# Kernel optimization log

Measured on AMD Instinct MI355X. Metric: run time of the kernel, lower is better.

Reference implementation:

```python
import jax, jax.numpy as jnp
import numpy as np

NUM_EXPERTS = 8
TOP_K = 2


def setup_inputs() -> dict:
    key = jax.random.key(0)
    ks = jax.random.split(key, 6)
    B, S, D, H, E = 4, 1024, 1024, 2048, NUM_EXPERTS
    x = jax.random.normal(ks[0], (B, S, D), dtype=jnp.float32)
    Wg = jax.random.normal(ks[1], (D, E), dtype=jnp.float32) * 0.02
    W1 = jax.random.normal(ks[2], (E, D, H), dtype=jnp.float32) * 0.02
    b1 = jax.random.normal(ks[3], (E, H), dtype=jnp.float32) * 0.02
    W2 = jax.random.normal(ks[4], (E, H, D), dtype=jnp.float32) * 0.02
    b2 = jax.random.normal(ks[5], (E, D), dtype=jnp.float32) * 0.02
    return {"x": x, "Wg": Wg, "W1": W1, "b1": b1, "W2": W2, "b2": b2}


def reference(x, Wg, W1, b1, W2, b2):
    B, S, D = x.shape
    E, _, H = W1.shape
    OUT = W2.shape[2]
    xm = x.reshape(-1, D)                      # [N, D], N = B*S
    # --- top-k gating (ProbabilitySamplerTopk): softmax over experts, take top-k ---
    logits = xm @ Wg                           # [N, E]
    probs = jax.nn.softmax(logits, axis=-1)
    topk_p, topk_i = jax.lax.top_k(probs, TOP_K)   # [N, K]
    # --- sort dispatched (token, expert) pairs by expert id (stable) ---
    flat_e = topk_i.reshape(-1)                # [N*K]
    flat_p = topk_p.reshape(-1)                # [N*K]
    order = jnp.argsort(flat_e)                # stable sort -> grouped by expert
    tok_idx = order // TOP_K                   # source token index (trunc-div by topK)
    e_sorted = flat_e[order]                   # [N*K]
    p_sorted = flat_p[order]                   # [N*K]
    xs = xm[tok_idx]                           # [N*K, D] expert-sorted inputs
    # --- grouped-GEMM experts: masked per-expert dense GEMM (E is small & fixed) ---
    y = jnp.zeros((xs.shape[0], OUT), dtype=xs.dtype)
    for e in range(E):
        h = jax.nn.relu(xs @ W1[e] + b1[e])    # [N*K, H]
        ye = h @ W2[e] + b2[e]                 # [N*K, OUT]
        m = (e_sorted == e)[:, None].astype(xs.dtype)
        y = y + m * ye
    # --- combine: multiply by gates, scatter-add back to token slots ---
    y = y * p_sorted[:, None]
    out = jnp.zeros((B * S, OUT), dtype=y.dtype).at[tok_idx].add(y)
    return out.reshape(B, S, OUT)
```

## Files before the change

### kernel.cpp

```cpp
#include <hip/hip_runtime.h>
#include <hip/hip_bf16.h>
#include <stdint.h>

typedef __bf16 bf16;
typedef __bf16 bf16x8 __attribute__((ext_vector_type(8)));
typedef __bf16 bf16x4 __attribute__((ext_vector_type(4)));
typedef float f32x4 __attribute__((ext_vector_type(4)));

#define N_TOK 4096
#define DDIM 1024
#define HDIM 2048
#define NPAIR 8192

__device__ __forceinline__ void gload16(const void* g, void* l) {
  __builtin_amdgcn_global_load_lds(
      (const __attribute__((address_space(1))) unsigned int*)g,
      (__attribute__((address_space(3))) unsigned int*)l, 16, 0, 0);
}

__global__ void transpose_cvt_kernel(const float* __restrict__ in, bf16* __restrict__ out,
                                     int R, int C) {
  __shared__ float tile[32][33];
  const float* ip = in + (size_t)blockIdx.z * R * C;
  bf16* op = out + (size_t)blockIdx.z * R * C;
  int r0 = blockIdx.y * 32, c0 = blockIdx.x * 32;
  int tr = threadIdx.x >> 3;
  int tc = (threadIdx.x & 7) * 4;
  float4 v = *(const float4*)(ip + (size_t)(r0 + tr) * C + c0 + tc);
  tile[tr][tc] = v.x; tile[tr][tc + 1] = v.y; tile[tr][tc + 2] = v.z; tile[tr][tc + 3] = v.w;
  __syncthreads();
  bf16x4 o = {(bf16)tile[tc + 0][tr], (bf16)tile[tc + 1][tr],
              (bf16)tile[tc + 2][tr], (bf16)tile[tc + 3][tr]};
  *(bf16x4*)(op + (size_t)(c0 + tr) * R + r0 + tc) = o;
}

__global__ void gate_kernel(const float* __restrict__ x, const float* __restrict__ Wg,
                            int2* __restrict__ ge, float2* __restrict__ gp,
                            bf16* __restrict__ xb, float* __restrict__ outp) {
  int t0 = blockIdx.x * 4;
  {
    float4 z = make_float4(0.f, 0.f, 0.f, 0.f);
    float4* ob = (float4*)(outp + (size_t)t0 * DDIM);
#pragma unroll
    for (int r = 0; r < 4; r++) ob[r * 256 + threadIdx.x] = z;
  }
  int t = t0 + (threadIdx.x >> 6);
  int lane = threadIdx.x & 63;
  const float* xr = x + (size_t)t * DDIM;
  bf16* xbr = xb + (size_t)t * DDIM;
  float a[8];
#pragma unroll
  for (int e = 0; e < 8; e++) a[e] = 0.f;
#pragma unroll
  for (int it = 0; it < 4; it++) {
    int d0 = it * 256 + lane * 4;
    float4 xv = *(const float4*)(xr + d0);
    bf16x4 o = {(bf16)xv.x, (bf16)xv.y, (bf16)xv.z, (bf16)xv.w};
    *(bf16x4*)(xbr + d0) = o;
    float xs[4] = {xv.x, xv.y, xv.z, xv.w};
#pragma unroll
    for (int dd = 0; dd < 4; dd++) {
      float4 w0 = *(const float4*)(Wg + (size_t)(d0 + dd) * 8);
      float4 w1 = *(const float4*)(Wg + (size_t)(d0 + dd) * 8 + 4);
      a[0] += xs[dd] * w0.x; a[1] += xs[dd] * w0.y; a[2] += xs[dd] * w0.z; a[3] += xs[dd] * w0.w;
      a[4] += xs[dd] * w1.x; a[5] += xs[dd] * w1.y; a[6] += xs[dd] * w1.z; a[7] += xs[dd] * w1.w;
    }
  }
#pragma unroll
  for (int off = 32; off >= 1; off >>= 1) {
#pragma unroll
    for (int e = 0; e < 8; e++) a[e] += __shfl_xor(a[e], off);
  }
  if (lane == 0) {
    float m = a[0];
#pragma unroll
    for (int e = 1; e < 8; e++) m = fmaxf(m, a[e]);
    float p[8]; float s = 0.f;
#pragma unroll
    for (int e = 0; e < 8; e++) { p[e] = expf(a[e] - m); s += p[e]; }
    float inv = 1.f / s;
    int i0 = 0; float v0 = a[0];
#pragma unroll
    for (int e = 1; e < 8; e++) if (a[e] > v0) { v0 = a[e]; i0 = e; }
    int i1 = -1; float v1 = -1e30f;
#pragma unroll
    for (int e = 0; e < 8; e++) if (e != i0 && a[e] > v1) { v1 = a[e]; i1 = e; }
    ge[t] = make_int2(i0, i1);
    gp[t] = make_float2(p[i0] * inv, p[i1] * inv);
  }
}

__global__ void sort_kernel(const int2* __restrict__ ge, const float2* __restrict__ gp,
                            int* __restrict__ tok, float* __restrict__ ps,
                            int* __restrict__ meta) {
  __shared__ int hist[8], runn[8], wc[16][8], wb[16][8], baseS[9];
  int tid = threadIdx.x;
  int lane = tid & 63, wv = tid >> 6;
  if (tid < 8) hist[tid] = 0;
  __syncthreads();
  for (int i = tid; i < NPAIR; i += 1024) {
    int2 g = ge[i >> 1];
    int e = (i & 1) ? g.y : g.x;
    atomicAdd(&hist[e], 1);
  }
  __syncthreads();
  if (tid == 0) {
    int b = 0, ts1 = 0;
    for (int e = 0; e < 8; e++) {
      baseS[e] = b; meta[e] = b;
      meta[9 + e] = ts1;  ts1 += (hist[e] + 127) / 128;
      b += hist[e];
    }
    baseS[8] = b; meta[8] = b; meta[17] = ts1;
  }
  __syncthreads();
  if (tid < 8) runn[tid] = baseS[tid];
  __syncthreads();
  for (int c = 0; c < 8; c++) {
    int i = c * 1024 + tid;
    int2 g = ge[i >> 1];
    int e = (i & 1) ? g.y : g.x;
    int rank = 0;
#pragma unroll
    for (int ee = 0; ee < 8; ee++) {
      unsigned long long b = __ballot(e == ee);
      if (e == ee) rank = __popcll(b & ((1ull << lane) - 1ull));
      if (lane == 0) wc[wv][ee] = __popcll(b);
    }
    __syncthreads();
    if (tid < 8) {
      int s = runn[tid];
      for (int w = 0; w < 16; w++) { wb[w][tid] = s; s += wc[w][tid]; }
      runn[tid] = s;
    }
    __syncthreads();
    int pos = wb[wv][e] + rank;
    tok[pos] = i >> 1;
    float2 p2 = gp[i >> 1];
    ps[pos] = (i & 1) ? p2.y : p2.x;
    __syncthreads();
  }
}

template <int KDIM, int NPE, bool FIRST, int NT>
__global__ __launch_bounds__(256, 4)
void moe_gemm_kernel(const bf16* __restrict__ A, const bf16* __restrict__ Bt,
                     const float* __restrict__ bias, const int* __restrict__ tok,
                     const float* __restrict__ ps, const int* __restrict__ meta,
                     bf16* __restrict__ hout, float* __restrict__ outp) {
  __shared__ bf16 lds[2][8192];
  constexpr int nk = KDIM / 32;

  int MTa = meta[17];
  int xcd = blockIdx.x & 7;
  int idx = blockIdx.x >> 3;
  int mLo = (MTa * xcd) >> 3;
  int mHi = (MTa * (xcd + 1)) >> 3;
  int cnt = mHi - mLo;
  if (idx >= cnt * NT) return;
  int tileN = idx / cnt;
  int tileM = mLo + idx - tileN * cnt;

  int e = 0;
#pragma unroll
  for (int k = 1; k < 8; k++) if (tileM >= meta[9 + k]) e = k;
  int row0 = meta[e] + (tileM - meta[9 + e]) * 128;
  int segEnd = meta[e + 1];
  int n0 = tileN * 128;

  int t = threadIdx.x;
  const bf16* aSrc[2];
  const bf16* bSrc[2];
  {
    int swz = ((t & 3) ^ ((t >> 3) & 3)) * 8;
#pragma unroll
    for (int r = 0; r < 2; r++) {
      int row = r * 64 + (t >> 2);
      int gRow = row0 + row; if (gRow > NPAIR - 1) gRow = NPAIR - 1;
      int arow = FIRST ? tok[gRow] : gRow;
      aSrc[r] = A + (size_t)arow * KDIM + swz;
      bSrc[r] = Bt + ((size_t)e * NPE + n0 + row) * KDIM + swz;
    }
  }

  int lane = t & 63, wv = t >> 6;
  int wm = wv >> 1, wn = wv & 1;
  int l15 = lane & 15, l4 = lane >> 4;
  int aOff[4], bOff[4];
#pragma unroll
  for (int m = 0; m < 4; m++) {
    int row = wm * 64 + m * 16 + l15;
    aOff[m] = row * 32 + ((l4 ^ ((row >> 1) & 3)) * 8);
  }
#pragma unroll
  for (int n = 0; n < 4; n++) {
    int row = wn * 64 + n * 16 + l15;
    bOff[n] = 4096 + row * 32 + ((l4 ^ ((row >> 1) & 3)) * 8);
  }

  f32x4 acc[4][4];
#pragma unroll
  for (int m = 0; m < 4; m++)
#pragma unroll
    for (int n = 0; n < 4; n++)
#pragma unroll
      for (int j = 0; j < 4; j++) acc[m][n][j] = 0.f;

  auto STAGE = [&](int kt, int buf) {
    bf16* sb = &lds[buf][0];
    int ko = kt * 32;
    gload16(aSrc[0] + ko, sb + t * 8);
    gload16(aSrc[1] + ko, sb + 2048 + t * 8);
    gload16(bSrc[0] + ko, sb + 4096 + t * 8);
    gload16(bSrc[1] + ko, sb + 6144 + t * 8);
  };

  STAGE(0, 0);
  __syncthreads();

  for (int kt = 0; kt < nk; kt++) {
    if (kt + 1 < nk) STAGE(kt + 1, (kt + 1) & 1);
    const bf16* sb = &lds[kt & 1][0];
    bf16x8 af[4], bfr[4];
#pragma unroll
    for (int m = 0; m < 4; m++) af[m] = *(const bf16x8*)(sb + aOff[m]);
#pragma unroll
    for (int n = 0; n < 4; n++) bfr[n] = *(const bf16x8*)(sb + bOff[n]);
#pragma unroll
    for (int m = 0; m < 4; m++)
#pragma unroll
      for (int n = 0; n < 4; n++)
        acc[m][n] = __builtin_amdgcn_mfma_f32_16x16x32_bf16(af[m], bfr[n], acc[m][n], 0, 0, 0);
    __syncthreads();
  }

  int colb = n0 + wn * 64 + l15;
  int rowb = wm * 64 + l4 * 4;
  float bia[4];
#pragma unroll
  for (int n = 0; n < 4; n++) bia[n] = bias[(size_t)e * NPE + colb + n * 16];
#pragma unroll
  for (int m = 0; m < 4; m++) {
#pragma unroll
    for (int jj = 0; jj < 4; jj++) {
      int gRow = row0 + rowb + m * 16 + jj;
      if (gRow < segEnd) {
        if (FIRST) {
#pragma unroll
          for (int n = 0; n < 4; n++) {
            float v = acc[m][n][jj] + bia[n];
            v = fmaxf(v, 0.f);
            hout[(size_t)gRow * NPE + colb + n * 16] = (bf16)v;
          }
        } else {
          float pscale = ps[gRow];
          float* orow = outp + (size_t)tok[gRow] * DDIM;
#pragma unroll
          for (int n = 0; n < 4; n++) {
            float v = (acc[m][n][jj] + bia[n]) * pscale;
            atomicAdd(orow + colb + n * 16, v);
          }
        }
      }
    }
  }
}

extern "C" void kernel_launch(void* const* d_in, const int* in_sizes, int n_in,
                              void* d_out, int out_size, void* d_ws, size_t ws_size,
                              hipStream_t stream) {
  (void)in_sizes; (void)n_in; (void)out_size; (void)ws_size;
  const float* x  = (const float*)d_in[0];
  const float* Wg = (const float*)d_in[1];
  const float* W1 = (const float*)d_in[2];
  const float* b1 = (const float*)d_in[3];
  const float* W2 = (const float*)d_in[4];
  const float* b2 = (const float*)d_in[5];
  float* out = (float*)d_out;

  char* ws = (char*)d_ws;
  bf16*  xb   = (bf16*)(ws);
  bf16*  W1T  = (bf16*)(ws + (8ull  << 20));
  bf16*  W2T  = (bf16*)(ws + (40ull << 20));
  bf16*  hbuf = (bf16*)(ws + (72ull << 20));
  char*  ext  = ws + (104ull << 20);
  int2*   ge      = (int2*)(ext);
  float2* gp      = (float2*)(ext + (64u  << 10));
  int*    tok     = (int*)(ext + (128u << 10));
  float*  psarr   = (float*)(ext + (160u << 10));
  int*    meta    = (int*)(ext + (224u << 10));

  transpose_cvt_kernel<<<dim3(64, 32, 8), 256, 0, stream>>>(W1, W1T, 1024, 2048);
  transpose_cvt_kernel<<<dim3(32, 64, 8), 256, 0, stream>>>(W2, W2T, 2048, 1024);
  gate_kernel<<<1024, 256, 0, stream>>>(x, Wg, ge, gp, xb, out);
  sort_kernel<<<1, 1024, 0, stream>>>(ge, gp, tok, psarr, meta);
  moe_gemm_kernel<1024, 2048, true, 16><<<dim3(1152), 256, 0, stream>>>(
      xb, W1T, b1, tok, psarr, meta, hbuf, nullptr);
  moe_gemm_kernel<2048, 1024, false, 8><<<dim3(576), 256, 0, stream>>>(
      hbuf, W2T, b2, tok, psarr, meta, nullptr, out);
}
```

Before: 194.5 us.

## Split second GEMM along K into two halves and load B directly from global

The second expert GEMM is split along K into two halves, which doubles its grid to the same block count as the first GEMM. Each half accumulates via atomics into its own fp32 buffer, and a new combine kernel adds the two buffers into the output. Both GEMMs now read B fragments straight from global memory into registers instead of staging them through LDS. This halves LDS use and the launch bound drops to 3 blocks. The trade-off is uncoalesced global B loads inside the inner loop, extra zeroing of two buffers, and an extra combine pass over the output.

After: 322.8 us. 1.66x slower.

```diff
diff --git a/kernel.cpp b/kernel.cpp
--- a/kernel.cpp
+++ b/kernel.cpp
@@ -36,13 +36,18 @@
 
 __global__ void gate_kernel(const float* __restrict__ x, const float* __restrict__ Wg,
                             int2* __restrict__ ge, float2* __restrict__ gp,
-                            bf16* __restrict__ xb, float* __restrict__ outp) {
+                            bf16* __restrict__ xb, float* __restrict__ y2a,
+                            float* __restrict__ y2b) {
   int t0 = blockIdx.x * 4;
   {
     float4 z = make_float4(0.f, 0.f, 0.f, 0.f);
-    float4* ob = (float4*)(outp + (size_t)t0 * DDIM);
-#pragma unroll
-    for (int r = 0; r < 4; r++) ob[r * 256 + threadIdx.x] = z;
+    float4* za = (float4*)(y2a + (size_t)t0 * DDIM);
+    float4* zb = (float4*)(y2b + (size_t)t0 * DDIM);
+#pragma unroll
+    for (int r = 0; r < 4; r++) {
+      za[r * 256 + threadIdx.x] = z;
+      zb[r * 256 + threadIdx.x] = z;
+    }
   }
   int t = t0 + (threadIdx.x >> 6);
   int lane = threadIdx.x & 63;
@@ -142,14 +147,19 @@
   }
 }
 
-template <int KDIM, int NPE, bool FIRST, int NT>
-__global__ __launch_bounds__(256, 4)
+template <bool FIRST>
+__global__ __launch_bounds__(256, 3)
 void moe_gemm_kernel(const bf16* __restrict__ A, const bf16* __restrict__ Bt,
                      const float* __restrict__ bias, const int* __restrict__ tok,
                      const float* __restrict__ ps, const int* __restrict__ meta,
-                     bf16* __restrict__ hout, float* __restrict__ outp) {
-  __shared__ bf16 lds[2][8192];
-  constexpr int nk = KDIM / 32;
+                     bf16* __restrict__ hout, float* __restrict__ y2a,
+                     float* __restrict__ y2b) {
+  constexpr int AKst = FIRST ? DDIM : HDIM;
+  constexpr int BKst = FIRST ? DDIM : HDIM;
+  constexpr int NPE  = FIRST ? HDIM : DDIM;
+  constexpr int NT   = 16;
+  constexpr int nk   = 32;
+  __shared__ bf16 lds[2][4096];
 
   int MTa = meta[17];
   int xcd = blockIdx.x & 7;
@@ -166,11 +176,12 @@
   for (int k = 1; k < 8; k++) if (tileM >= meta[9 + k]) e = k;
   int row0 = meta[e] + (tileM - meta[9 + e]) * 128;
   int segEnd = meta[e + 1];
-  int n0 = tileN * 128;
+  int n0, kOff;
+  if (FIRST) { n0 = tileN * 128; kOff = 0; }
+  else       { n0 = (tileN & 7) * 128; kOff = (tileN >> 3) * 1024; }
 
   int t = threadIdx.x;
   const bf16* aSrc[2];
-  const bf16* bSrc[2];
   {
     int swz = ((t & 3) ^ ((t >> 3) & 3)) * 8;
 #pragma unroll
@@ -178,24 +189,24 @@
       int row = r * 64 + (t >> 2);
       int gRow = row0 + row; if (gRow > NPAIR - 1) gRow = NPAIR - 1;
       int arow = FIRST ? tok[gRow] : gRow;
-      aSrc[r] = A + (size_t)arow * KDIM + swz;
-      bSrc[r] = Bt + ((size_t)e * NPE + n0 + row) * KDIM + swz;
+      aSrc[r] = A + (size_t)arow * AKst + kOff + swz;
     }
   }
 
   int lane = t & 63, wv = t >> 6;
   int wm = wv >> 1, wn = wv & 1;
   int l15 = lane & 15, l4 = lane >> 4;
-  int aOff[4], bOff[4];
+  int aOff[4];
 #pragma unroll
   for (int m = 0; m < 4; m++) {
     int row = wm * 64 + m * 16 + l15;
     aOff[m] = row * 32 + ((l4 ^ ((row >> 1) & 3)) * 8);
   }
+  const bf16* bBase[4];
 #pragma unroll
   for (int n = 0; n < 4; n++) {
     int row = wn * 64 + n * 16 + l15;
-    bOff[n] = 4096 + row * 32 + ((l4 ^ ((row >> 1) & 3)) * 8);
+    bBase[n] = Bt + ((size_t)e * NPE + n0 + row) * BKst + kOff + l4 * 8;
   }
 
   f32x4 acc[4][4];
@@ -206,26 +217,24 @@
 #pragma unroll
       for (int j = 0; j < 4; j++) acc[m][n][j] = 0.f;
 
-  auto STAGE = [&](int kt, int buf) {
+  auto STAGE_A = [&](int kt, int buf) {
     bf16* sb = &lds[buf][0];
     int ko = kt * 32;
     gload16(aSrc[0] + ko, sb + t * 8);
     gload16(aSrc[1] + ko, sb + 2048 + t * 8);
-    gload16(bSrc[0] + ko, sb + 4096 + t * 8);
-    gload16(bSrc[1] + ko, sb + 6144 + t * 8);
   };
 
-  STAGE(0, 0);
+  STAGE_A(0, 0);
   __syncthreads();
 
   for (int kt = 0; kt < nk; kt++) {
-    if (kt + 1 < nk) STAGE(kt + 1, (kt + 1) & 1);
+    if (kt + 1 < nk) STAGE_A(kt + 1, (kt + 1) & 1);
     const bf16* sb = &lds[kt & 1][0];
     bf16x8 af[4], bfr[4];
 #pragma unroll
+    for (int n = 0; n < 4; n++) bfr[n] = *(const bf16x8*)(bBase[n] + kt * 32);
+#pragma unroll
     for (int m = 0; m < 4; m++) af[m] = *(const bf16x8*)(sb + aOff[m]);
-#pragma unroll
-    for (int n = 0; n < 4; n++) bfr[n] = *(const bf16x8*)(sb + bOff[n]);
 #pragma unroll
     for (int m = 0; m < 4; m++)
 #pragma unroll
@@ -238,7 +247,9 @@
   int rowb = wm * 64 + l4 * 4;
   float bia[4];
 #pragma unroll
-  for (int n = 0; n < 4; n++) bia[n] = bias[(size_t)e * NPE + colb + n * 16];
+  for (int n = 0; n < 4; n++)
+    bia[n] = (FIRST || kOff == 0) ? bias[(size_t)e * NPE + colb + n * 16] : 0.f;
+  float* ybuf = FIRST ? nullptr : ((kOff == 0) ? y2a : y2b);
 #pragma unroll
   for (int m = 0; m < 4; m++) {
 #pragma unroll
@@ -250,11 +261,11 @@
           for (int n = 0; n < 4; n++) {
             float v = acc[m][n][jj] + bia[n];
             v = fmaxf(v, 0.f);
-            hout[(size_t)gRow * NPE + colb + n * 16] = (bf16)v;
+            hout[(size_t)gRow * HDIM + colb + n * 16] = (bf16)v;
           }
         } else {
           float pscale = ps[gRow];
-          float* orow = outp + (size_t)tok[gRow] * DDIM;
+          float* orow = ybuf + (size_t)tok[gRow] * DDIM;
 #pragma unroll
           for (int n = 0; n < 4; n++) {
             float v = (acc[m][n][jj] + bia[n]) * pscale;
@@ -264,6 +275,14 @@
       }
     }
   }
+}
+
+__global__ void combine_kernel(const float* __restrict__ a, const float* __restrict__ b,
+                               float* __restrict__ out) {
+  int i = blockIdx.x * 256 + threadIdx.x;
+  f32x4 va = ((const f32x4*)a)[i];
+  f32x4 vb = ((const f32x4*)b)[i];
+  ((f32x4*)out)[i] = va + vb;
 }
 
 extern "C" void kernel_launch(void* const* d_in, const int* in_sizes, int n_in,
@@ -283,7 +302,9 @@
   bf16*  W1T  = (bf16*)(ws + (8ull  << 20));
   bf16*  W2T  = (bf16*)(ws + (40ull << 20));
   bf16*  hbuf = (bf16*)(ws + (72ull << 20));
-  char*  ext  = ws + (104ull << 20);
+  float* y2a  = (float*)(ws + (104ull << 20));
+  float* y2b  = (float*)(ws + (120ull << 20));
+  char*  ext  = ws + (136ull << 20);
   int2*   ge      = (int2*)(ext);
   float2* gp      = (float2*)(ext + (64u  << 10));
   int*    tok     = (int*)(ext + (128u << 10));
@@ -292,10 +313,11 @@
 
   transpose_cvt_kernel<<<dim3(64, 32, 8), 256, 0, stream>>>(W1, W1T, 1024, 2048);
   transpose_cvt_kernel<<<dim3(32, 64, 8), 256, 0, stream>>>(W2, W2T, 2048, 1024);
-  gate_kernel<<<1024, 256, 0, stream>>>(x, Wg, ge, gp, xb, out);
+  gate_kernel<<<1024, 256, 0, stream>>>(x, Wg, ge, gp, xb, y2a, y2b);
   sort_kernel<<<1, 1024, 0, stream>>>(ge, gp, tok, psarr, meta);
-  moe_gemm_kernel<1024, 2048, true, 16><<<dim3(1152), 256, 0, stream>>>(
-      xb, W1T, b1, tok, psarr, meta, hbuf, nullptr);
-  moe_gemm_kernel<2048, 1024, false, 8><<<dim3(576), 256, 0, stream>>>(
-      hbuf, W2T, b2, tok, psarr, meta, nullptr, out);
-}
+  moe_gemm_kernel<true><<<dim3(1152), 256, 0, stream>>>(
+      xb, W1T, b1, tok, psarr, meta, hbuf, nullptr, nullptr);
+  moe_gemm_kernel<false><<<dim3(1152), 256, 0, stream>>>(
+      hbuf, W2T, b2, tok, psarr, meta, nullptr, y2a, y2b);
+  combine_kernel<<<4096, 256, 0, stream>>>(y2a, y2b, out);
+}
```

## Use 32x32x16 MFMA in expert GEMMs and widen transpose tiles to 64x64

Applied to the files above, without the earlier changes.

The grouped expert GEMM inner loop moves from 16x16x32 bf16 MFMA instructions to 32x32x16 ones, so each wave issues four larger MFMAs per k-substep from fewer LDS fragment loads. The epilogue is remapped to the 32x32 accumulator layout. Separately, the weight transpose/convert kernel now processes 64x64 tiles per block and writes 16-byte bf16x8 stores. This reduces LDS read traffic per FLOP and improves transpose store width, at the cost of a larger LDS tile and a more complex output index mapping.

Result: slower. 205.1 us (+5.5%).

```diff
diff --git a/kernel.cpp b/kernel.cpp
--- a/kernel.cpp
+++ b/kernel.cpp
@@ -6,6 +6,7 @@
 typedef __bf16 bf16x8 __attribute__((ext_vector_type(8)));
 typedef __bf16 bf16x4 __attribute__((ext_vector_type(4)));
 typedef float f32x4 __attribute__((ext_vector_type(4)));
+typedef float f32x16 __attribute__((ext_vector_type(16)));
 
 #define N_TOK 4096
 #define DDIM 1024
@@ -18,20 +19,34 @@
       (__attribute__((address_space(3))) unsigned int*)l, 16, 0, 0);
 }
 
-__global__ void transpose_cvt_kernel(const float* __restrict__ in, bf16* __restrict__ out,
-                                     int R, int C) {
-  __shared__ float tile[32][33];
+__global__ __launch_bounds__(256)
+void transpose_cvt_kernel(const float* __restrict__ in, bf16* __restrict__ out,
+                          int R, int C) {
+  __shared__ float tile[64][65];
   const float* ip = in + (size_t)blockIdx.z * R * C;
   bf16* op = out + (size_t)blockIdx.z * R * C;
-  int r0 = blockIdx.y * 32, c0 = blockIdx.x * 32;
-  int tr = threadIdx.x >> 3;
-  int tc = (threadIdx.x & 7) * 4;
-  float4 v = *(const float4*)(ip + (size_t)(r0 + tr) * C + c0 + tc);
-  tile[tr][tc] = v.x; tile[tr][tc + 1] = v.y; tile[tr][tc + 2] = v.z; tile[tr][tc + 3] = v.w;
-  __syncthreads();
-  bf16x4 o = {(bf16)tile[tc + 0][tr], (bf16)tile[tc + 1][tr],
-              (bf16)tile[tc + 2][tr], (bf16)tile[tc + 3][tr]};
-  *(bf16x4*)(op + (size_t)(c0 + tr) * R + r0 + tc) = o;
+  int c0 = blockIdx.x * 64, r0 = blockIdx.y * 64;
+  int t = threadIdx.x;
+  int ir = t >> 2;
+  int icb = (t & 3) * 16;
+#pragma unroll
+  for (int j = 0; j < 4; j++) {
+    float4 v = *(const float4*)(ip + (size_t)(r0 + ir) * C + c0 + icb + j * 4);
+    tile[ir][icb + j * 4 + 0] = v.x;
+    tile[ir][icb + j * 4 + 1] = v.y;
+    tile[ir][icb + j * 4 + 2] = v.z;
+    tile[ir][icb + j * 4 + 3] = v.w;
+  }
+  __syncthreads();
+  int oc = t >> 2;
+  int orb = (t & 3) * 16;
+#pragma unroll
+  for (int s = 0; s < 2; s++) {
+    bf16x8 o;
+#pragma unroll
+    for (int q = 0; q < 8; q++) o[q] = (bf16)tile[orb + s * 8 + q][oc];
+    *(bf16x8*)(op + (size_t)(c0 + oc) * R + r0 + orb + s * 8) = o;
+  }
 }
 
 __global__ void gate_kernel(const float* __restrict__ x, const float* __restrict__ Wg,
@@ -185,26 +200,26 @@
 
   int lane = t & 63, wv = t >> 6;
   int wm = wv >> 1, wn = wv & 1;
-  int l15 = lane & 15, l4 = lane >> 4;
-  int aOff[4], bOff[4];
-#pragma unroll
-  for (int m = 0; m < 4; m++) {
-    int row = wm * 64 + m * 16 + l15;
-    aOff[m] = row * 32 + ((l4 ^ ((row >> 1) & 3)) * 8);
-  }
-#pragma unroll
-  for (int n = 0; n < 4; n++) {
-    int row = wn * 64 + n * 16 + l15;
-    bOff[n] = 4096 + row * 32 + ((l4 ^ ((row >> 1) & 3)) * 8);
-  }
-
-  f32x4 acc[4][4];
-#pragma unroll
-  for (int m = 0; m < 4; m++)
-#pragma unroll
-    for (int n = 0; n < 4; n++)
-#pragma unroll
-      for (int j = 0; j < 4; j++) acc[m][n][j] = 0.f;
+  int l31 = lane & 31, l5 = lane >> 5;
+  int aOff[2][2], bOff[2][2];
+#pragma unroll
+  for (int f = 0; f < 2; f++)
+#pragma unroll
+    for (int ks = 0; ks < 2; ks++) {
+      int arow = wm * 64 + f * 32 + l31;
+      int brow = wn * 64 + f * 32 + l31;
+      int kc = ks * 2 + l5;
+      aOff[f][ks] = arow * 32 + ((kc ^ ((arow >> 1) & 3)) * 8);
+      bOff[f][ks] = 4096 + brow * 32 + ((kc ^ ((brow >> 1) & 3)) * 8);
+    }
+
+  f32x16 acc[2][2];
+#pragma unroll
+  for (int m = 0; m < 2; m++)
+#pragma unroll
+    for (int n = 0; n < 2; n++)
+#pragma unroll
+      for (int j = 0; j < 16; j++) acc[m][n][j] = 0.f;
 
   auto STAGE = [&](int kt, int buf) {
     bf16* sb = &lds[buf][0];
@@ -221,44 +236,49 @@
   for (int kt = 0; kt < nk; kt++) {
     if (kt + 1 < nk) STAGE(kt + 1, (kt + 1) & 1);
     const bf16* sb = &lds[kt & 1][0];
-    bf16x8 af[4], bfr[4];
-#pragma unroll
-    for (int m = 0; m < 4; m++) af[m] = *(const bf16x8*)(sb + aOff[m]);
-#pragma unroll
-    for (int n = 0; n < 4; n++) bfr[n] = *(const bf16x8*)(sb + bOff[n]);
-#pragma unroll
-    for (int m = 0; m < 4; m++)
-#pragma unroll
-      for (int n = 0; n < 4; n++)
-        acc[m][n] = __builtin_amdgcn_mfma_f32_16x16x32_bf16(af[m], bfr[n], acc[m][n], 0, 0, 0);
+#pragma unroll
+    for (int ks = 0; ks < 2; ks++) {
+      bf16x8 af[2], bfr[2];
+#pragma unroll
+      for (int f = 0; f < 2; f++) {
+        af[f] = *(const bf16x8*)(sb + aOff[f][ks]);
+        bfr[f] = *(const bf16x8*)(sb + bOff[f][ks]);
+      }
+#pragma unroll
+      for (int m = 0; m < 2; m++)
+#pragma unroll
+        for (int n = 0; n < 2; n++)
+          acc[m][n] = __builtin_amdgcn_mfma_f32_32x32x16_bf16(af[m], bfr[n], acc[m][n], 0, 0, 0);
+    }
     __syncthreads();
   }
 
-  int colb = n0 + wn * 64 + l15;
-  int rowb = wm * 64 + l4 * 4;
-  float bia[4];
-#pragma unroll
-  for (int n = 0; n < 4; n++) bia[n] = bias[(size_t)e * NPE + colb + n * 16];
-#pragma unroll
-  for (int m = 0; m < 4; m++) {
-#pragma unroll
-    for (int jj = 0; jj < 4; jj++) {
-      int gRow = row0 + rowb + m * 16 + jj;
+  float bia[2];
+#pragma unroll
+  for (int n = 0; n < 2; n++)
+    bia[n] = bias[(size_t)e * NPE + n0 + wn * 64 + n * 32 + l31];
+#pragma unroll
+  for (int m = 0; m < 2; m++) {
+#pragma unroll
+    for (int r = 0; r < 16; r++) {
+      int crow = (r & 3) + 8 * (r >> 2) + 4 * l5;
+      int gRow = row0 + wm * 64 + m * 32 + crow;
       if (gRow < segEnd) {
         if (FIRST) {
 #pragma unroll
-          for (int n = 0; n < 4; n++) {
-            float v = acc[m][n][jj] + bia[n];
-            v = fmaxf(v, 0.f);
-            hout[(size_t)gRow * NPE + colb + n * 16] = (bf16)v;
+          for (int n = 0; n < 2; n++) {
+            int col = n0 + wn * 64 + n * 32 + l31;
+            float v = acc[m][n][r] + bia[n];
+            hout[(size_t)gRow * NPE + col] = (bf16)fmaxf(v, 0.f);
           }
         } else {
           float pscale = ps[gRow];
           float* orow = outp + (size_t)tok[gRow] * DDIM;
 #pragma unroll
-          for (int n = 0; n < 4; n++) {
-            float v = (acc[m][n][jj] + bia[n]) * pscale;
-            atomicAdd(orow + colb + n * 16, v);
+          for (int n = 0; n < 2; n++) {
+            int col = n0 + wn * 64 + n * 32 + l31;
+            float v = (acc[m][n][r] + bia[n]) * pscale;
+            atomicAdd(orow + col, v);
           }
         }
       }
@@ -290,8 +310,8 @@
   float*  psarr   = (float*)(ext + (160u << 10));
   int*    meta    = (int*)(ext + (224u << 10));
 
-  transpose_cvt_kernel<<<dim3(64, 32, 8), 256, 0, stream>>>(W1, W1T, 1024, 2048);
-  transpose_cvt_kernel<<<dim3(32, 64, 8), 256, 0, stream>>>(W2, W2T, 2048, 1024);
+  transpose_cvt_kernel<<<dim3(32, 16, 8), 256, 0, stream>>>(W1, W1T, 1024, 2048);
+  transpose_cvt_kernel<<<dim3(16, 32, 8), 256, 0, stream>>>(W2, W2T, 2048, 1024);
   gate_kernel<<<1024, 256, 0, stream>>>(x, Wg, ge, gp, xb, out);
   sort_kernel<<<1, 1024, 0, stream>>>(ge, gp, tok, psarr, meta);
   moe_gemm_kernel<1024, 2048, true, 16><<<dim3(1152), 256, 0, stream>>>(
```
